# Performance work log

Hardware: AMD Instinct MI355X
Metric: run time of the kernel (lower is better)

## Reference

```python
import jax, jax.numpy as jnp
import numpy as np

EPSILON = 1e-8

def setup_inputs() -> dict:
    key = jax.random.key(0)
    k1, k2, k3, k4 = jax.random.split(key, 4)
    B, C_in, C_out, H, W, S, K = 16, 512, 512, 32, 32, 512, 3
    x = jax.random.normal(k1, (B, C_in, H, W), dtype=jnp.float32)
    w = jax.random.normal(k2, (B, S), dtype=jnp.float32)
    # Linear(style_dim -> in_chan), bias initialized to ones per module code
    style_w = jax.random.normal(k3, (C_in, S), dtype=jnp.float32) * (1.0 / np.sqrt(S))
    style_b = jnp.ones((C_in,), dtype=jnp.float32)
    # kaiming_normal_(fan_in, leaky_relu): std = sqrt(2/(1+0.01^2)) / sqrt(fan_in)
    fan_in = C_in * K * K
    gain = np.sqrt(2.0 / (1.0 + 0.01 ** 2))
    weight = jax.random.normal(k4, (C_out, C_in, K, K), dtype=jnp.float32) * (gain / np.sqrt(fan_in))
    return {"x": x, "w": w, "style_w": style_w, "style_b": style_b, "weight": weight}

def reference(x, w, style_w, style_b, weight):
    B, C, H, W_ = x.shape
    C_out, _, K, _ = weight.shape
    # style modulation: Linear(style_dim -> in_chan)
    style = w @ style_w.T + style_b                       # (B, C_in)
    weights = style[:, None, :, None, None] * weight[None]  # (B, C_out, C_in, K, K)
    # demodulation
    d = jax.lax.rsqrt(jnp.sum(weights * weights, axis=(2, 3, 4), keepdims=True) + EPSILON)
    weights = weights * d
    # grouped conv with groups = batch
    pad = 1 if K > 1 else 0
    xg = x.reshape(1, B * C, H, W_)
    wg = weights.reshape(B * C_out, C, K, K)
    y = jax.lax.conv_general_dilated(
        xg, wg, window_strides=(1, 1), padding=((pad, pad), (pad, pad)),
        dimension_numbers=("NCHW", "OIHW", "NCHW"), feature_group_count=B)
    return y.reshape(B, C_out, H, W_)
```

## Files before the change

### kernel.cpp

```cpp
#include <hip/hip_runtime.h>
#include <hip/hip_bf16.h>

#define NB 16
#define CI 512
#define CO 512
#define HW 1024
#define SD 512
#define EPSI 1e-8f

typedef __attribute__((ext_vector_type(8))) short bf16x8;
typedef __attribute__((ext_vector_type(16))) float f32x16;
typedef __attribute__((ext_vector_type(4))) unsigned int u32x4;

#define GLOAD_LDS16(g, l) __builtin_amdgcn_global_load_lds( \
    (const __attribute__((address_space(1))) unsigned int*)(const void*)(g), \
    (__attribute__((address_space(3))) unsigned int*)(void*)(l), 16, 0, 0)
#define SCHED0() __builtin_amdgcn_sched_barrier(0)
#define SBAR()   __builtin_amdgcn_s_barrier()

__global__ void k_prep(const float* __restrict__ w, const float* __restrict__ sw,
                       const float* __restrict__ sb, const float* __restrict__ wt,
                       float* __restrict__ style, float* __restrict__ wsq,
                       __hip_bfloat16* __restrict__ wtb, u32x4* __restrict__ zpage) {
    if (blockIdx.x < 2048) {
        int gw = (blockIdx.x * 256 + threadIdx.x) >> 6;
        int l = threadIdx.x & 63;
        int b = gw >> 9, c = gw & 511;
        const float4* wr = (const float4*)(w + b * SD) + (l << 1);
        const float4* sr = (const float4*)(sw + c * SD) + (l << 1);
        float4 a0 = wr[0], a1 = wr[1], q0 = sr[0], q1 = sr[1];
        float acc = a0.x * q0.x + a0.y * q0.y + a0.z * q0.z + a0.w * q0.w
                  + a1.x * q1.x + a1.y * q1.y + a1.z * q1.z + a1.w * q1.w;
#pragma unroll
        for (int off = 32; off > 0; off >>= 1) acc += __shfl_down(acc, off);
        if (l == 0) style[gw] = acc + sb[c];
    } else {
        if (blockIdx.x == 2048 && threadIdx.x < 64)
            zpage[threadIdx.x] = (u32x4){0, 0, 0, 0};
        int idx = (blockIdx.x - 2048) * 256 + threadIdx.x;
        const float* p = wt + idx * 9;
        float a = 0.f;
#pragma unroll
        for (int t = 0; t < 9; ++t) {
            float v = p[t];
            a += v * v;
            wtb[t * (CO * CI) + idx] = __float2bfloat16(v);
        }
        wsq[idx] = a;
    }
}

__global__ void k_xs(const float* __restrict__ x, const float* __restrict__ style,
                     __hip_bfloat16* __restrict__ xs) {
    __shared__ float tile[32][66];
    int b = blockIdx.z, c0 = blockIdx.y * 64, p0 = blockIdx.x * 32;
    int tx = threadIdx.x & 31, ty = threadIdx.x >> 5;
#pragma unroll
    for (int i = 0; i < 8; ++i) {
        int ci = i * 8 + ty;
        tile[tx][ci] = x[((size_t)b * CI + c0 + ci) * HW + p0 + tx] * style[b * CI + c0 + ci];
    }
    __syncthreads();
    int r = threadIdx.x >> 3, kc = threadIdx.x & 7;
    union { bf16x8 v; __hip_bfloat16 h[8]; } U;
#pragma unroll
    for (int i = 0; i < 8; ++i)
        U.h[i] = __float2bfloat16(tile[r][kc * 8 + i]);
    *(bf16x8*)(xs + ((size_t)b * HW + p0 + r) * CI + c0 + kc * 8) = U.v;
}

#define XS_BYTES 52224
#define WBUF_BYTES 16384
#define DV_OFF (2 * XS_BYTES + 3 * WBUF_BYTES)
#define SMEM_TOTAL (DV_OFF + 1024)

extern "C" __global__ __launch_bounds__(512, 2) void k_conv(
        const __hip_bfloat16* __restrict__ wtb,
        const __hip_bfloat16* __restrict__ xs,
        const float* __restrict__ style,
        const float* __restrict__ wsq,
        const char* __restrict__ zpage,
        float* __restrict__ out) {
    extern __shared__ char smem[];
    char* Xs  = smem;
    char* Wsb = smem + 2 * XS_BYTES;
    float* dvLDS = (float*)(smem + DV_OFF);

    const int tid  = threadIdx.x;
    const int lane = tid & 63;
    const int wv   = tid >> 6;
    const int wb   = wv >> 2;
    const int wr   = (wv >> 1) & 1;
    const int wn   = wv & 1;

    int bid = blockIdx.x;
    int xcd = bid & 7, idx = bid >> 3;
    int cot = xcd >> 1;
    int px8 = idx & 7;
    int bp  = (idx >> 3) | ((xcd & 1) << 2);
    const int co0 = cot * 128;
    const int p0  = px8 * 128;
    const int y0  = px8 * 4;
    const int b0  = bp * 2;
    const int b   = b0 + wb;

    if (tid < 192) {
        int g = tid & 7;
        int rx = ((tid >> 3) & 1) ? 33 : 0;
        int row = tid >> 4;
        int off = (row * 34 + rx) * 128 + g * 16;
        *(u32x4*)(Xs + off) = (u32x4){0, 0, 0, 0};
        *(u32x4*)(Xs + XS_BYTES + off) = (u32x4){0, 0, 0, 0};
    }

    const int srcgW = (lane & 7) ^ (lane >> 3);

    auto issueW = [&](int tap, int cin, int bufi) {
        const __hip_bfloat16* wsrc = wtb + ((size_t)tap * CO + co0) * CI + cin;
        char* wdst = Wsb + bufi * WBUF_BYTES;
#pragma unroll
        for (int k = 0; k < 2; ++k) {
            int seg = k * 8 + wv;
            int co_l = seg * 8 + (lane >> 3);
            GLOAD_LDS16(wsrc + co_l * CI + srcgW * 8, wdst + seg * 1024);
        }
    };
    auto issueX = [&](char* Xdst, int cin) {
#pragma unroll
        for (int k = 0; k < 6; ++k) {
            int sid = k * 8 + wv;
            int bb = (sid >= 24) ? 1 : 0;
            int rem = sid - bb * 24;
            int ry = rem >> 2, seg = rem & 3;
            int rx0 = 1 + seg * 8;
            char* ldst = Xdst + ((bb * 6 + ry) * 34 + rx0) * 128;
            int y = y0 - 1 + ry;
            int rx = rx0 + (lane >> 3);
            int srcg = (lane & 7) ^ (rx & 7);
            if ((unsigned)y < 32u)
                GLOAD_LDS16(xs + ((size_t)(b0 + bb) * HW + (y << 5) + (rx - 1)) * CI + cin + srcg * 8, ldst);
            else
                GLOAD_LDS16(zpage, ldst);
        }
    };

    f32x16 acc[2][2];
#pragma unroll
    for (int m = 0; m < 2; ++m)
#pragma unroll
        for (int n = 0; n < 2; ++n)
            acc[m][n] = (f32x16)(0.f);

    issueW(0, 0, 0);
    issueW(1, 0, 1);
    issueX(Xs, 0);
    {
        int idx2 = tid >> 1, h = tid & 1;
        int bb = idx2 >> 7, col = idx2 & 127;
        const float4* wq = (const float4*)(wsq + (size_t)(co0 + col) * CI) + h * 64;
        const float4* st = (const float4*)(style + (size_t)(b0 + bb) * CI) + h * 64;
        float a = 0.f;
#pragma unroll 4
        for (int i = 0; i < 64; ++i) {
            float4 q = wq[i], s = st[i];
            a += s.x * s.x * q.x + s.y * s.y * q.y + s.z * s.z * q.z + s.w * s.w * q.w;
        }
        a += __shfl_down(a, 1);
        if (!h) dvLDS[idx2] = rsqrtf(a + EPSI);
    }
    SCHED0();
    asm volatile("s_waitcnt lgkmcnt(0) vmcnt(0)" ::: "memory");
    SCHED0();
    SBAR();
    SCHED0();

    for (int cc = 0; cc < 8; ++cc) {
        const char* Xcur = Xs + (cc & 1) * XS_BYTES;
#pragma unroll
        for (int t = 0; t < 9; ++t) {
            if (!(cc == 7 && t >= 7)) {
                const int tn  = (t <= 6) ? (t + 2) : (t - 7);
                const int cin = ((t <= 6) ? cc : (cc + 1)) * 64;
                issueW(tn, cin, (t + 2) % 3);
            }
            if (t == 0 && cc < 7)
                issueX(Xs + ((cc + 1) & 1) * XS_BYTES, (cc + 1) * 64);
            SCHED0();

            const char* Wb = Wsb + (t % 3) * WBUF_BYTES;
            const int ky = t / 3, kx = t - (t / 3) * 3;
            __builtin_amdgcn_s_setprio(1);
#pragma unroll
            for (int q = 0; q < 4; ++q) {
                bf16x8 afr[2], bfr[2];
                int g = (q << 1) + (lane >> 5);
#pragma unroll
                for (int m = 0; m < 2; ++m) {
                    int cr = wr * 64 + m * 32 + (lane & 31);
                    afr[m] = *(const bf16x8*)(Wb + cr * 128 + ((g ^ (cr & 7)) << 4));
                }
#pragma unroll
                for (int n = 0; n < 2; ++n) {
                    int ry = wn * 2 + n + ky;
                    int rx = (lane & 31) + kx;
                    bfr[n] = *(const bf16x8*)(Xcur + ((wb * 6 + ry) * 34 + rx) * 128 +
                                              ((g ^ (rx & 7)) << 4));
                }
#pragma unroll
                for (int m = 0; m < 2; ++m)
#pragma unroll
                    for (int n = 0; n < 2; ++n)
                        acc[m][n] = __builtin_amdgcn_mfma_f32_32x32x16_bf16(afr[m], bfr[n], acc[m][n], 0, 0, 0);
            }
            __builtin_amdgcn_s_setprio(0);

            if (!(cc == 7 && t == 8)) {
                SCHED0();
                if (cc < 7 && t < 2)
                    asm volatile("s_waitcnt lgkmcnt(0) vmcnt(8)" ::: "memory");
                else if (cc == 7 && t == 7)
                    asm volatile("s_waitcnt lgkmcnt(0) vmcnt(0)" ::: "memory");
                else
                    asm volatile("s_waitcnt lgkmcnt(0) vmcnt(2)" ::: "memory");
                SCHED0();
                SBAR();
                SCHED0();
            }
        }
    }

#pragma unroll
    for (int m = 0; m < 2; ++m) {
#pragma unroll
        for (int r = 0; r < 16; ++r) {
            int col = wr * 64 + m * 32 + (r & 3) + ((r >> 2) << 3) + ((lane >> 5) << 2);
            float dvv = dvLDS[wb * 128 + col];
            float* orow = out + ((size_t)b * CO + co0 + col) * HW + p0 + wn * 64;
            orow[lane & 31]        = acc[m][0][r] * dvv;
            orow[32 + (lane & 31)] = acc[m][1][r] * dvv;
        }
    }
}

extern "C" void kernel_launch(void* const* d_in, const int* in_sizes, int n_in,
                              void* d_out, int out_size, void* d_ws, size_t ws_size,
                              hipStream_t stream) {
    const float* x  = (const float*)d_in[0];
    const float* w  = (const float*)d_in[1];
    const float* sw = (const float*)d_in[2];
    const float* sb = (const float*)d_in[3];
    const float* wt = (const float*)d_in[4];
    float* out = (float*)d_out;

    char* ws = (char*)d_ws;
    float* style = (float*)(ws);
    float* wsq   = (float*)(ws + 65536);
    __hip_bfloat16* wtb = (__hip_bfloat16*)(ws + 1114112);
    __hip_bfloat16* xsb = (__hip_bfloat16*)(ws + 5832704);
    char* zpage = ws + 22609920;

    hipFuncSetAttribute((const void*)k_conv,
                        hipFuncAttributeMaxDynamicSharedMemorySize, SMEM_TOTAL);

    k_prep<<<3072, 256, 0, stream>>>(w, sw, sb, wt, style, wsq,
                                     (__hip_bfloat16*)wtb, (u32x4*)zpage);
    k_xs<<<dim3(32, 8, 16), 256, 0, stream>>>(x, style, xsb);
    k_conv<<<256, 512, SMEM_TOTAL, stream>>>(wtb, xsb, style, wsq, zpage, out);
}
```

Baseline: 109.0 us.

## Load conv weights directly into registers in MFMA fragment layout, one batch per block

Repacks the bf16 weights in the prep kernel into an MFMA-fragment-friendly layout so the conv kernel can load A fragments straight from global memory into registers. Weights are double-buffered in registers across taps rather than staged through LDS. This drops the per-tap barriers, keeping only one barrier per input-channel chunk. Each block now handles one batch with 256 threads (512 blocks) using half the LDS, and demodulation moves to a separate kernel. The trade-offs are more register pressure, global-load latency exposed per tap, less weight reuse across batches within a block, and an extra kernel launch.

```diff
diff --git a/kernel.cpp b/kernel.cpp
--- a/kernel.cpp
+++ b/kernel.cpp
@@ -21,7 +21,7 @@
 __global__ void k_prep(const float* __restrict__ w, const float* __restrict__ sw,
                        const float* __restrict__ sb, const float* __restrict__ wt,
                        float* __restrict__ style, float* __restrict__ wsq,
-                       __hip_bfloat16* __restrict__ wtb, u32x4* __restrict__ zpage) {
+                       __hip_bfloat16* __restrict__ wtb2) {
     if (blockIdx.x < 2048) {
         int gw = (blockIdx.x * 256 + threadIdx.x) >> 6;
         int l = threadIdx.x & 63;
@@ -35,19 +35,33 @@
         for (int off = 32; off > 0; off >>= 1) acc += __shfl_down(acc, off);
         if (l == 0) style[gw] = acc + sb[c];
     } else {
-        if (blockIdx.x == 2048 && threadIdx.x < 64)
-            zpage[threadIdx.x] = (u32x4){0, 0, 0, 0};
         int idx = (blockIdx.x - 2048) * 256 + threadIdx.x;
-        const float* p = wt + idx * 9;
+        int co = idx >> 9, ci = idx & 511;
+        const float* p = wt + (size_t)idx * 9;
         float a = 0.f;
 #pragma unroll
         for (int t = 0; t < 9; ++t) {
             float v = p[t];
             a += v * v;
-            wtb[t * (CO * CI) + idx] = __float2bfloat16(v);
+            wtb2[(((size_t)t * 64 + (ci >> 3)) * CO + co) * 8 + (ci & 7)] = __float2bfloat16(v);
         }
         wsq[idx] = a;
     }
+}
+
+__global__ void k_demod2(const float* __restrict__ style, const float* __restrict__ wsq,
+                         float* __restrict__ dv) {
+    int gw = (blockIdx.x * 256 + threadIdx.x) >> 6;
+    int l = threadIdx.x & 63;
+    int b = gw >> 9, co = gw & 511;
+    const float4* st = (const float4*)(style + b * CI) + (l << 1);
+    const float4* wq = (const float4*)(wsq + (size_t)co * CI) + (l << 1);
+    float4 s0 = st[0], s1 = st[1], q0 = wq[0], q1 = wq[1];
+    float acc = s0.x * s0.x * q0.x + s0.y * s0.y * q0.y + s0.z * s0.z * q0.z + s0.w * s0.w * q0.w
+              + s1.x * s1.x * q1.x + s1.y * s1.y * q1.y + s1.z * s1.z * q1.z + s1.w * s1.w * q1.w;
+#pragma unroll
+    for (int off = 32; off > 0; off >>= 1) acc += __shfl_down(acc, off);
+    if (l == 0) dv[gw] = rsqrtf(acc + EPSI);
 }
 
 __global__ void k_xs(const float* __restrict__ x, const float* __restrict__ style,
@@ -69,78 +83,98 @@
     *(bf16x8*)(xs + ((size_t)b * HW + p0 + r) * CI + c0 + kc * 8) = U.v;
 }
 
-#define XS_BYTES 52224
-#define WBUF_BYTES 16384
-#define DV_OFF (2 * XS_BYTES + 3 * WBUF_BYTES)
-#define SMEM_TOTAL (DV_OFF + 1024)
-
-extern "C" __global__ __launch_bounds__(512, 2) void k_conv(
-        const __hip_bfloat16* __restrict__ wtb,
+#define XS_BYTES 26112
+#define SMEM_TOTAL (2 * XS_BYTES)
+
+#define TAP(T, WCUR, WNXT)                                                       \
+    {                                                                            \
+        constexpr int T_ = (T);                                                  \
+        if (cc * 9 + T_ < 71)                                                    \
+            loadW((T_ == 8) ? 0 : T_ + 1, (T_ == 8) ? cc + 1 : cc, WNXT);        \
+        constexpr int ky = T_ / 3, kx = T_ % 3;                                  \
+        __builtin_amdgcn_s_setprio(1);                                           \
+        _Pragma("unroll")                                                        \
+        for (int q = 0; q < 4; ++q) {                                            \
+            bf16x8 bfr[2];                                                       \
+            int g = (q << 1) + (lane >> 5);                                      \
+            _Pragma("unroll")                                                    \
+            for (int n = 0; n < 2; ++n) {                                        \
+                int rx = (lane & 31) + kx;                                       \
+                bfr[n] = *(const bf16x8*)(Xcur + ((wn * 2 + n + ky) * 34 + rx) * 128 + \
+                                          ((g ^ (rx & 7)) << 4));                \
+            }                                                                    \
+            _Pragma("unroll")                                                    \
+            for (int m = 0; m < 2; ++m)                                          \
+                _Pragma("unroll")                                                \
+                for (int n = 0; n < 2; ++n)                                      \
+                    acc[m][n] = __builtin_amdgcn_mfma_f32_32x32x16_bf16(         \
+                        WCUR[q * 2 + m], bfr[n], acc[m][n], 0, 0, 0);            \
+        }                                                                        \
+        __builtin_amdgcn_s_setprio(0);                                           \
+    }
+
+extern "C" __global__ __launch_bounds__(256, 2) void k_conv(
+        const __hip_bfloat16* __restrict__ wtb2,
         const __hip_bfloat16* __restrict__ xs,
-        const float* __restrict__ style,
-        const float* __restrict__ wsq,
-        const char* __restrict__ zpage,
+        const float* __restrict__ dvec,
         float* __restrict__ out) {
     extern __shared__ char smem[];
-    char* Xs  = smem;
-    char* Wsb = smem + 2 * XS_BYTES;
-    float* dvLDS = (float*)(smem + DV_OFF);
+    char* Xs = smem;
 
     const int tid  = threadIdx.x;
     const int lane = tid & 63;
+    const int l31  = lane & 31;
     const int wv   = tid >> 6;
-    const int wb   = wv >> 2;
-    const int wr   = (wv >> 1) & 1;
+    const int wr   = wv >> 1;
     const int wn   = wv & 1;
 
     int bid = blockIdx.x;
     int xcd = bid & 7, idx = bid >> 3;
-    int cot = xcd >> 1;
-    int px8 = idx & 7;
-    int bp  = (idx >> 3) | ((xcd & 1) << 2);
+    const int cot = xcd >> 1;
+    const int px8 = idx & 7;
+    const int b   = (idx >> 3) | ((xcd & 1) << 3);
     const int co0 = cot * 128;
     const int p0  = px8 * 128;
     const int y0  = px8 * 4;
-    const int b0  = bp * 2;
-    const int b   = b0 + wb;
 
     if (tid < 192) {
-        int g = tid & 7;
-        int rx = ((tid >> 3) & 1) ? 33 : 0;
-        int row = tid >> 4;
-        int off = (row * 34 + rx) * 128 + g * 16;
-        *(u32x4*)(Xs + off) = (u32x4){0, 0, 0, 0};
-        *(u32x4*)(Xs + XS_BYTES + off) = (u32x4){0, 0, 0, 0};
-    }
-
-    const int srcgW = (lane & 7) ^ (lane >> 3);
-
-    auto issueW = [&](int tap, int cin, int bufi) {
-        const __hip_bfloat16* wsrc = wtb + ((size_t)tap * CO + co0) * CI + cin;
-        char* wdst = Wsb + bufi * WBUF_BYTES;
-#pragma unroll
-        for (int k = 0; k < 2; ++k) {
-            int seg = k * 8 + wv;
-            int co_l = seg * 8 + (lane >> 3);
-            GLOAD_LDS16(wsrc + co_l * CI + srcgW * 8, wdst + seg * 1024);
-        }
+        int bufi = tid / 96, r = tid % 96;
+        int g = r & 7;
+        int rx = (r & 8) ? 33 : 0;
+        int row = r >> 4;
+        *(u32x4*)(Xs + bufi * XS_BYTES + (row * 34 + rx) * 128 + g * 16) = (u32x4){0, 0, 0, 0};
+    }
+
+    int woff[4][2];
+#pragma unroll
+    for (int q = 0; q < 4; ++q)
+#pragma unroll
+        for (int m = 0; m < 2; ++m)
+            woff[q][m] = (((q << 1) + (lane >> 5)) * CO + wr * 64 + m * 32 + l31) * 8;
+
+    auto loadW = [&](int tp, int c8, bf16x8 (&dst)[8]) {
+        const __hip_bfloat16* wsrc = wtb2 + ((size_t)(tp * 64 + c8 * 8) * CO + co0) * 8;
+#pragma unroll
+        for (int q = 0; q < 4; ++q)
+#pragma unroll
+            for (int m = 0; m < 2; ++m)
+                dst[q * 2 + m] = *(const bf16x8*)(wsrc + woff[q][m]);
     };
+
     auto issueX = [&](char* Xdst, int cin) {
 #pragma unroll
         for (int k = 0; k < 6; ++k) {
-            int sid = k * 8 + wv;
-            int bb = (sid >= 24) ? 1 : 0;
-            int rem = sid - bb * 24;
-            int ry = rem >> 2, seg = rem & 3;
+            int sid = k * 4 + wv;
+            int ry = sid >> 2, seg = sid & 3;
             int rx0 = 1 + seg * 8;
-            char* ldst = Xdst + ((bb * 6 + ry) * 34 + rx0) * 128;
+            char* ldst = Xdst + (ry * 34 + rx0) * 128;
             int y = y0 - 1 + ry;
             int rx = rx0 + (lane >> 3);
             int srcg = (lane & 7) ^ (rx & 7);
             if ((unsigned)y < 32u)
-                GLOAD_LDS16(xs + ((size_t)(b0 + bb) * HW + (y << 5) + (rx - 1)) * CI + cin + srcg * 8, ldst);
+                GLOAD_LDS16(xs + ((size_t)b * HW + (y << 5) + (rx - 1)) * CI + cin + srcg * 8, ldst);
             else
-                GLOAD_LDS16(zpage, ldst);
+                *(u32x4*)(ldst + (lane << 4)) = (u32x4){0, 0, 0, 0};
         }
     };
 
@@ -151,81 +185,35 @@
         for (int n = 0; n < 2; ++n)
             acc[m][n] = (f32x16)(0.f);
 
-    issueW(0, 0, 0);
-    issueW(1, 0, 1);
+    bf16x8 wfA[8], wfB[8];
+
+    loadW(0, 0, wfA);
     issueX(Xs, 0);
-    {
-        int idx2 = tid >> 1, h = tid & 1;
-        int bb = idx2 >> 7, col = idx2 & 127;
-        const float4* wq = (const float4*)(wsq + (size_t)(co0 + col) * CI) + h * 64;
-        const float4* st = (const float4*)(style + (size_t)(b0 + bb) * CI) + h * 64;
-        float a = 0.f;
-#pragma unroll 4
-        for (int i = 0; i < 64; ++i) {
-            float4 q = wq[i], s = st[i];
-            a += s.x * s.x * q.x + s.y * s.y * q.y + s.z * s.z * q.z + s.w * s.w * q.w;
-        }
-        a += __shfl_down(a, 1);
-        if (!h) dvLDS[idx2] = rsqrtf(a + EPSI);
-    }
     SCHED0();
-    asm volatile("s_waitcnt lgkmcnt(0) vmcnt(0)" ::: "memory");
+    asm volatile("s_waitcnt vmcnt(0) lgkmcnt(0)" ::: "memory");
     SCHED0();
     SBAR();
     SCHED0();
 
     for (int cc = 0; cc < 8; ++cc) {
         const char* Xcur = Xs + (cc & 1) * XS_BYTES;
-#pragma unroll
-        for (int t = 0; t < 9; ++t) {
-            if (!(cc == 7 && t >= 7)) {
-                const int tn  = (t <= 6) ? (t + 2) : (t - 7);
-                const int cin = ((t <= 6) ? cc : (cc + 1)) * 64;
-                issueW(tn, cin, (t + 2) % 3);
-            }
-            if (t == 0 && cc < 7)
-                issueX(Xs + ((cc + 1) & 1) * XS_BYTES, (cc + 1) * 64);
+        if (cc < 7)
+            issueX(Xs + ((cc + 1) & 1) * XS_BYTES, (cc + 1) * 64);
+        if (!(cc & 1)) {
+            TAP(0, wfA, wfB) TAP(1, wfB, wfA) TAP(2, wfA, wfB)
+            TAP(3, wfB, wfA) TAP(4, wfA, wfB) TAP(5, wfB, wfA)
+            TAP(6, wfA, wfB) TAP(7, wfB, wfA) TAP(8, wfA, wfB)
+        } else {
+            TAP(0, wfB, wfA) TAP(1, wfA, wfB) TAP(2, wfB, wfA)
+            TAP(3, wfA, wfB) TAP(4, wfB, wfA) TAP(5, wfA, wfB)
+            TAP(6, wfB, wfA) TAP(7, wfA, wfB) TAP(8, wfB, wfA)
+        }
+        if (cc < 7) {
             SCHED0();
-
-            const char* Wb = Wsb + (t % 3) * WBUF_BYTES;
-            const int ky = t / 3, kx = t - (t / 3) * 3;
-            __builtin_amdgcn_s_setprio(1);
-#pragma unroll
-            for (int q = 0; q < 4; ++q) {
-                bf16x8 afr[2], bfr[2];
-                int g = (q << 1) + (lane >> 5);
-#pragma unroll
-                for (int m = 0; m < 2; ++m) {
-                    int cr = wr * 64 + m * 32 + (lane & 31);
-                    afr[m] = *(const bf16x8*)(Wb + cr * 128 + ((g ^ (cr & 7)) << 4));
-                }
-#pragma unroll
-                for (int n = 0; n < 2; ++n) {
-                    int ry = wn * 2 + n + ky;
-                    int rx = (lane & 31) + kx;
-                    bfr[n] = *(const bf16x8*)(Xcur + ((wb * 6 + ry) * 34 + rx) * 128 +
-                                              ((g ^ (rx & 7)) << 4));
-                }
-#pragma unroll
-                for (int m = 0; m < 2; ++m)
-#pragma unroll
-                    for (int n = 0; n < 2; ++n)
-                        acc[m][n] = __builtin_amdgcn_mfma_f32_32x32x16_bf16(afr[m], bfr[n], acc[m][n], 0, 0, 0);
-            }
-            __builtin_amdgcn_s_setprio(0);
-
-            if (!(cc == 7 && t == 8)) {
-                SCHED0();
-                if (cc < 7 && t < 2)
-                    asm volatile("s_waitcnt lgkmcnt(0) vmcnt(8)" ::: "memory");
-                else if (cc == 7 && t == 7)
-                    asm volatile("s_waitcnt lgkmcnt(0) vmcnt(0)" ::: "memory");
-                else
-                    asm volatile("s_waitcnt lgkmcnt(0) vmcnt(2)" ::: "memory");
-                SCHED0();
-                SBAR();
-                SCHED0();
-            }
+            asm volatile("s_waitcnt vmcnt(0) lgkmcnt(0)" ::: "memory");
+            SCHED0();
+            SBAR();
+            SCHED0();
         }
     }
 
@@ -234,10 +222,10 @@
 #pragma unroll
         for (int r = 0; r < 16; ++r) {
             int col = wr * 64 + m * 32 + (r & 3) + ((r >> 2) << 3) + ((lane >> 5) << 2);
-            float dvv = dvLDS[wb * 128 + col];
+            float dvv = dvec[b * CO + co0 + col];
             float* orow = out + ((size_t)b * CO + co0 + col) * HW + p0 + wn * 64;
-            orow[lane & 31]        = acc[m][0][r] * dvv;
-            orow[32 + (lane & 31)] = acc[m][1][r] * dvv;
+            orow[l31]      = acc[m][0][r] * dvv;
+            orow[32 + l31] = acc[m][1][r] * dvv;
         }
     }
 }
@@ -254,16 +242,16 @@
 
     char* ws = (char*)d_ws;
     float* style = (float*)(ws);
+    float* dvec  = (float*)(ws + 32768);
     float* wsq   = (float*)(ws + 65536);
-    __hip_bfloat16* wtb = (__hip_bfloat16*)(ws + 1114112);
-    __hip_bfloat16* xsb = (__hip_bfloat16*)(ws + 5832704);
-    char* zpage = ws + 22609920;
+    __hip_bfloat16* wtb2 = (__hip_bfloat16*)(ws + 1114112);
+    __hip_bfloat16* xsb  = (__hip_bfloat16*)(ws + 5832704);
 
     hipFuncSetAttribute((const void*)k_conv,
                         hipFuncAttributeMaxDynamicSharedMemorySize, SMEM_TOTAL);
 
-    k_prep<<<3072, 256, 0, stream>>>(w, sw, sb, wt, style, wsq,
-                                     (__hip_bfloat16*)wtb, (u32x4*)zpage);
+    k_prep<<<3072, 256, 0, stream>>>(w, sw, sb, wt, style, wsq, (__hip_bfloat16*)wtb2);
     k_xs<<<dim3(32, 8, 16), 256, 0, stream>>>(x, style, xsb);
-    k_conv<<<256, 512, SMEM_TOTAL, stream>>>(wtb, xsb, style, wsq, zpage, out);
-}
+    k_demod2<<<2048, 256, 0, stream>>>(style, wsq, dvec);
+    k_conv<<<512, 256, SMEM_TOTAL, stream>>>(wtb2, xsb, dvec, out);
+}
```

Result: slower. 224.6 us (+106.0%).
